# Performance work log

Measured on AMD Instinct MI355X. Metric: run time of the kernel, lower is better.

Reference implementation:

```python
import jax, jax.numpy as jnp
import numpy as np

B, N, F, D = 8, 2048, 128, 128


def setup_inputs() -> dict:
    key = jax.random.key(0)
    k1, k2, k3 = jax.random.split(key, 3)
    inputs = jax.random.normal(k1, (B, N, F), dtype=jnp.float32)
    adj = jax.random.uniform(k2, (B, N, N), dtype=jnp.float32)  # nonneg weights -> positive degrees
    W_kernel = jax.random.normal(k3, (F, D), dtype=jnp.float32) * (1.0 / np.sqrt(F))
    W_bias = jnp.zeros((D,), dtype=jnp.float32)
    return {"inputs": inputs, "adj": adj, "W_kernel": W_kernel, "W_bias": W_bias}


def _normalize_adjacency(adj):
    # D^{-1/2} A D^{-1/2}: same math as diag-matmul chain, via broadcast scaling
    d = jnp.sum(adj, axis=-1)                      # [B, N]
    d_sqrt_inv = jnp.power(d, -0.5)
    d_sqrt_inv = jnp.where(jnp.isinf(d_sqrt_inv), 0.0, d_sqrt_inv)
    return d_sqrt_inv[..., :, None] * adj * d_sqrt_inv[..., None, :]


def reference(inputs, adj, W_kernel, W_bias):
    adj_norm = _normalize_adjacency(adj)           # [B, N, N]
    feats = inputs @ W_kernel + W_bias             # [B, N, D]
    out = jnp.einsum('bnm,bmd->bnd', adj_norm, feats)
    return jax.nn.relu(out)
```

## Files before the change

### kernel.cpp

```cpp
#include <hip/hip_runtime.h>
#include <hip/hip_bf16.h>
#include <stdint.h>

#define B_ 8
#define N_ 2048
#define F_ 128
#define D_ 128

typedef short bf16x8 __attribute__((ext_vector_type(8)));
typedef float f32x4 __attribute__((ext_vector_type(4)));

__device__ __forceinline__ unsigned short f2bf(float f) {
    unsigned u = __float_as_uint(f);
    u += 0x7fffu + ((u >> 16) & 1u);
    return (unsigned short)(u >> 16);
}

__global__ __launch_bounds__(256) void k_degwt(const float* __restrict__ adj,
                                               const float* __restrict__ W,
                                               float* __restrict__ rs,
                                               unsigned short* __restrict__ Wt) {
    if (blockIdx.x < 4096) {
        const int wave = threadIdx.x >> 6, lane = threadIdx.x & 63;
        const int row = blockIdx.x * 4 + wave;
        const float4* p = (const float4*)(adj + (size_t)row * N_);
        float s = 0.f;
#pragma unroll
        for (int j = 0; j < 8; ++j) {
            float4 v = p[j * 64 + lane];
            s += (v.x + v.y) + (v.z + v.w);
        }
#pragma unroll
        for (int m = 1; m < 64; m <<= 1) s += __shfl_xor(s, m, 64);
        if (lane == 0) rs[row] = (s > 0.f) ? (1.0f / sqrtf(s)) : 0.f;
    } else {
        int c = (blockIdx.x - 4096) * 256 + threadIdx.x;
        int d = c >> 4, f0 = (c & 15) * 8;
        union { bf16x8 v; unsigned short u[8]; } pk;
#pragma unroll
        for (int e = 0; e < 8; ++e) pk.u[e] = f2bf(W[(size_t)(f0 + e) * D_ + d]);
        *(bf16x8*)(Wt + (size_t)d * F_ + f0) = pk.v;
    }
}

__global__ __launch_bounds__(256) void k_feat(const float* __restrict__ x,
                                              const unsigned short* __restrict__ Wt,
                                              const float* __restrict__ bias,
                                              unsigned short* __restrict__ gt) {
    __shared__ __align__(16) unsigned char sX[64 * 128 * 2];
    __shared__ __align__(16) unsigned char sW[128 * 128 * 2];
    const int t = threadIdx.x;
    const int R0 = blockIdx.x * 64;

#pragma unroll
    for (int j = 0; j < 8; ++j) {
        int c = j * 256 + t;
        unsigned L = (unsigned)c * 16u;
        unsigned lg = L ^ (((L >> 8) & 7u) << 4);
        const unsigned char* src = (const unsigned char*)Wt + lg;
        __builtin_amdgcn_global_load_lds(
            (const __attribute__((address_space(1))) void*)src,
            (__attribute__((address_space(3))) void*)(sW + L), 16, 0, 0);
    }
#pragma unroll
    for (int j = 0; j < 4; ++j) {
        int c = j * 256 + t;
        int row = c >> 4, sub = c & 15;
        const float4* src = (const float4*)(x + (size_t)(R0 + row) * F_ + sub * 8);
        float4 v0 = src[0], v1 = src[1];
        union { bf16x8 v; unsigned short u[8]; } pk;
        pk.u[0] = f2bf(v0.x); pk.u[1] = f2bf(v0.y); pk.u[2] = f2bf(v0.z); pk.u[3] = f2bf(v0.w);
        pk.u[4] = f2bf(v1.x); pk.u[5] = f2bf(v1.y); pk.u[6] = f2bf(v1.z); pk.u[7] = f2bf(v1.w);
        unsigned byte = (unsigned)(row * 256 + sub * 16);
        byte ^= ((byte >> 8) & 7u) << 4;
        *(bf16x8*)(sX + byte) = pk.v;
    }
    __syncthreads();

    const int w = t >> 6, l = t & 63, lr = l & 15, lh = l >> 4;
    f32x4 acc[8];
#pragma unroll
    for (int j = 0; j < 8; ++j) acc[j] = (f32x4){0.f, 0.f, 0.f, 0.f};

#pragma unroll
    for (int ks = 0; ks < 4; ++ks) {
        int f0 = lh * 8 + ks * 32;
        unsigned abyte = (unsigned)((w * 16 + lr) * 256 + f0 * 2);
        abyte ^= ((abyte >> 8) & 7u) << 4;
        bf16x8 a = *(const bf16x8*)(sX + abyte);
#pragma unroll
        for (int j = 0; j < 8; ++j) {
            unsigned bbyte = (unsigned)((j * 16 + lr) * 256 + f0 * 2);
            bbyte ^= ((bbyte >> 8) & 7u) << 4;
            bf16x8 bb = *(const bf16x8*)(sW + bbyte);
            acc[j] = __builtin_amdgcn_mfma_f32_16x16x32_bf16(a, bb, acc[j], 0, 0, 0);
        }
    }

#pragma unroll
    for (int j = 0; j < 8; ++j) {
        int d = j * 16 + lr;
        float bv = bias[d];
#pragma unroll
        for (int r = 0; r < 4; ++r) {
            int m = R0 + w * 16 + lh * 4 + r;
            float v = acc[j][r] + bv;
            int b = m >> 11, n = m & (N_ - 1);
            gt[((size_t)b * D_ + d) * N_ + n] = f2bf(v);
        }
    }
}

__global__ __launch_bounds__(512) void k_gcn(const float* __restrict__ adj,
                                             const unsigned short* __restrict__ gt,
                                             const float* __restrict__ rs,
                                             float* __restrict__ out) {
    __shared__ __align__(16) unsigned char sA[2][32 * 128 * 2];
    __shared__ __align__(16) unsigned char sB[2][128 * 128 * 2];

    unsigned bid = blockIdx.x;
    unsigned wg = (bid & 7u) * 64u + (bid >> 3);
    const int b = (int)(wg >> 6);
    const int nt = (int)(wg & 63u);
    const int R0 = nt * 32;

    const float* adjB = adj + (size_t)b * N_ * N_ + (size_t)R0 * N_;
    const unsigned short* gtB = gt + (size_t)b * D_ * N_;
    const float* rsB = rs + b * N_;

    const int t = threadIdx.x;
    const int w = t >> 6, l = t & 63, lr = l & 15, lh = l >> 4;
    const int wr = (w >> 2) * 16, wc = (w & 3) * 32;

    auto stage = [&](int bufidx, int k0) {
        unsigned char* sBb = sB[bufidx];
#pragma unroll
        for (int i = 0; i < 4; ++i) {
            int c = i * 512 + t;
            unsigned L = (unsigned)c * 16u;
            unsigned lg = L ^ (((L >> 8) & 7u) << 4);
            int d = (int)(lg >> 8);
            int mloc = (int)(lg & 255u) >> 1;
            const unsigned short* g = gtB + (size_t)d * N_ + k0 + mloc;
            __builtin_amdgcn_global_load_lds(
                (const __attribute__((address_space(1))) void*)g,
                (__attribute__((address_space(3))) void*)(sBb + L), 16, 0, 0);
        }
        {
            int row = t >> 4, sub = t & 15;
            const float4* src = (const float4*)(adjB + (size_t)row * N_ + k0 + sub * 8);
            const float4* rsm = (const float4*)(rsB + k0 + sub * 8);
            float4 v0 = src[0], v1 = src[1];
            float4 r0 = rsm[0], r1 = rsm[1];
            union { bf16x8 v; unsigned short u[8]; } pk;
            pk.u[0] = f2bf(v0.x * r0.x); pk.u[1] = f2bf(v0.y * r0.y);
            pk.u[2] = f2bf(v0.z * r0.z); pk.u[3] = f2bf(v0.w * r0.w);
            pk.u[4] = f2bf(v1.x * r1.x); pk.u[5] = f2bf(v1.y * r1.y);
            pk.u[6] = f2bf(v1.z * r1.z); pk.u[7] = f2bf(v1.w * r1.w);
            unsigned byte = (unsigned)(row * 256 + sub * 16);
            byte ^= ((byte >> 8) & 7u) << 4;
            *(bf16x8*)(sA[bufidx] + byte) = pk.v;
        }
    };

    f32x4 acc[2];
    acc[0] = (f32x4){0.f, 0.f, 0.f, 0.f};
    acc[1] = (f32x4){0.f, 0.f, 0.f, 0.f};

    stage(0, 0);
    __syncthreads();

    const int NITER = N_ / 128;
    for (int it = 0; it < NITER; ++it) {
        int cur = it & 1;
        if (it + 1 < NITER) stage(cur ^ 1, (it + 1) * 128);

        const unsigned char* pA = sA[cur];
        const unsigned char* pB = sB[cur];
#pragma unroll
        for (int kk = 0; kk < 4; ++kk) {
            unsigned abyte = (unsigned)((wr + lr) * 256 + lh * 16 + kk * 64);
            abyte ^= ((abyte >> 8) & 7u) << 4;
            bf16x8 a = *(const bf16x8*)(pA + abyte);
#pragma unroll
            for (int jn = 0; jn < 2; ++jn) {
                int d = wc + jn * 16 + lr;
                unsigned bbyte = (unsigned)(d * 256 + lh * 16 + kk * 64);
                bbyte ^= ((bbyte >> 8) & 7u) << 4;
                bf16x8 bb = *(const bf16x8*)(pB + bbyte);
                acc[jn] = __builtin_amdgcn_mfma_f32_16x16x32_bf16(a, bb, acc[jn], 0, 0, 0);
            }
        }
        __syncthreads();
    }

#pragma unroll
    for (int r = 0; r < 4; ++r) {
        int row = wr + lh * 4 + r;
        float rsn = rsB[R0 + row];
#pragma unroll
        for (int jn = 0; jn < 2; ++jn) {
            int d = wc + jn * 16 + lr;
            float v = acc[jn][r] * rsn;
            out[((size_t)(b * N_ + R0 + row)) * D_ + d] = fmaxf(v, 0.f);
        }
    }
}

extern "C" void kernel_launch(void* const* d_in, const int* in_sizes, int n_in,
                              void* d_out, int out_size, void* d_ws, size_t ws_size,
                              hipStream_t stream) {
    const float* inputs = (const float*)d_in[0];
    const float* adj    = (const float*)d_in[1];
    const float* Wk     = (const float*)d_in[2];
    const float* Wb     = (const float*)d_in[3];
    float* out = (float*)d_out;

    float* rs = (float*)d_ws;
    unsigned short* gt = (unsigned short*)((char*)d_ws + 65536);
    unsigned short* Wt = (unsigned short*)((char*)d_ws + 65536 + (size_t)B_ * D_ * N_ * 2);

    k_degwt<<<4096 + 8, 256, 0, stream>>>(adj, Wk, rs, Wt);
    k_feat <<<(B_ * N_) / 64, 256, 0, stream>>>(inputs, Wt, Wb, gt);
    k_gcn  <<<B_ * (N_ / 32), 512, 0, stream>>>(adj, gt, rs, out);
}
```

Measured before the change: 56.73 us.

## Fold column degree scaling into features and split K across waves in GCN matmul

The column-side D^{-1/2} scaling now happens once in the feature kernel, where it is applied to the projected features before they are stored as bf16. This removes the per-tile rs loads and multiplies from the adjacency staging path. The main kernel also changes its wave split: each wave now covers a 32x32 output tile over half of the K slice per iteration, loading two A and two B fragments for four MFMAs, which raises fragment reuse. The two K-halves are reduced through shared memory at the end, which adds an extra barrier and LDS traffic. Rounding to bf16 after scaling changes numerics slightly.

```diff
diff --git a/kernel.cpp b/kernel.cpp
--- a/kernel.cpp
+++ b/kernel.cpp
@@ -46,6 +46,7 @@
 __global__ __launch_bounds__(256) void k_feat(const float* __restrict__ x,
                                               const unsigned short* __restrict__ Wt,
                                               const float* __restrict__ bias,
+                                              const float* __restrict__ rs,
                                               unsigned short* __restrict__ gt) {
     __shared__ __align__(16) unsigned char sX[64 * 128 * 2];
     __shared__ __align__(16) unsigned char sW[128 * 128 * 2];
@@ -84,29 +85,30 @@
 
 #pragma unroll
     for (int ks = 0; ks < 4; ++ks) {
-        int f0 = lh * 8 + ks * 32;
-        unsigned abyte = (unsigned)((w * 16 + lr) * 256 + f0 * 2);
+        unsigned abyte = (unsigned)((w * 16 + lr) * 256 + lh * 16 + ks * 64);
         abyte ^= ((abyte >> 8) & 7u) << 4;
         bf16x8 a = *(const bf16x8*)(sX + abyte);
 #pragma unroll
         for (int j = 0; j < 8; ++j) {
-            unsigned bbyte = (unsigned)((j * 16 + lr) * 256 + f0 * 2);
+            unsigned bbyte = (unsigned)((j * 16 + lr) * 256 + lh * 16 + ks * 64);
             bbyte ^= ((bbyte >> 8) & 7u) << 4;
             bf16x8 bb = *(const bf16x8*)(sW + bbyte);
             acc[j] = __builtin_amdgcn_mfma_f32_16x16x32_bf16(a, bb, acc[j], 0, 0, 0);
         }
     }
 
+    const int m0 = R0 + w * 16 + lh * 4;
+    float4 r4 = *(const float4*)(rs + m0);
+    float rr[4] = {r4.x, r4.y, r4.z, r4.w};
 #pragma unroll
     for (int j = 0; j < 8; ++j) {
         int d = j * 16 + lr;
         float bv = bias[d];
 #pragma unroll
         for (int r = 0; r < 4; ++r) {
-            int m = R0 + w * 16 + lh * 4 + r;
-            float v = acc[j][r] + bv;
+            int m = m0 + r;
             int b = m >> 11, n = m & (N_ - 1);
-            gt[((size_t)b * D_ + d) * N_ + n] = f2bf(v);
+            gt[((size_t)b * D_ + d) * N_ + n] = f2bf((acc[j][r] + bv) * rr[r]);
         }
     }
 }
@@ -121,16 +123,15 @@
     unsigned bid = blockIdx.x;
     unsigned wg = (bid & 7u) * 64u + (bid >> 3);
     const int b = (int)(wg >> 6);
-    const int nt = (int)(wg & 63u);
-    const int R0 = nt * 32;
+    const int R0 = (int)(wg & 63u) * 32;
 
     const float* adjB = adj + (size_t)b * N_ * N_ + (size_t)R0 * N_;
     const unsigned short* gtB = gt + (size_t)b * D_ * N_;
-    const float* rsB = rs + b * N_;
+    const float* rsB = rs + (size_t)b * N_;
 
     const int t = threadIdx.x;
     const int w = t >> 6, l = t & 63, lr = l & 15, lh = l >> 4;
-    const int wr = (w >> 2) * 16, wc = (w & 3) * 32;
+    const int kg = w >> 2, cg = w & 3;
 
     auto stage = [&](int bufidx, int k0) {
         unsigned char* sBb = sB[bufidx];
@@ -149,23 +150,23 @@
         {
             int row = t >> 4, sub = t & 15;
             const float4* src = (const float4*)(adjB + (size_t)row * N_ + k0 + sub * 8);
-            const float4* rsm = (const float4*)(rsB + k0 + sub * 8);
             float4 v0 = src[0], v1 = src[1];
-            float4 r0 = rsm[0], r1 = rsm[1];
             union { bf16x8 v; unsigned short u[8]; } pk;
-            pk.u[0] = f2bf(v0.x * r0.x); pk.u[1] = f2bf(v0.y * r0.y);
-            pk.u[2] = f2bf(v0.z * r0.z); pk.u[3] = f2bf(v0.w * r0.w);
-            pk.u[4] = f2bf(v1.x * r1.x); pk.u[5] = f2bf(v1.y * r1.y);
-            pk.u[6] = f2bf(v1.z * r1.z); pk.u[7] = f2bf(v1.w * r1.w);
+            pk.u[0] = f2bf(v0.x); pk.u[1] = f2bf(v0.y);
+            pk.u[2] = f2bf(v0.z); pk.u[3] = f2bf(v0.w);
+            pk.u[4] = f2bf(v1.x); pk.u[5] = f2bf(v1.y);
+            pk.u[6] = f2bf(v1.z); pk.u[7] = f2bf(v1.w);
             unsigned byte = (unsigned)(row * 256 + sub * 16);
             byte ^= ((byte >> 8) & 7u) << 4;
             *(bf16x8*)(sA[bufidx] + byte) = pk.v;
         }
     };
 
-    f32x4 acc[2];
-    acc[0] = (f32x4){0.f, 0.f, 0.f, 0.f};
-    acc[1] = (f32x4){0.f, 0.f, 0.f, 0.f};
+    f32x4 acc[2][2];
+#pragma unroll
+    for (int i = 0; i < 2; ++i)
+#pragma unroll
+        for (int jn = 0; jn < 2; ++jn) acc[i][jn] = (f32x4){0.f, 0.f, 0.f, 0.f};
 
     stage(0, 0);
     __syncthreads();
@@ -178,31 +179,60 @@
         const unsigned char* pA = sA[cur];
         const unsigned char* pB = sB[cur];
 #pragma unroll
-        for (int kk = 0; kk < 4; ++kk) {
-            unsigned abyte = (unsigned)((wr + lr) * 256 + lh * 16 + kk * 64);
-            abyte ^= ((abyte >> 8) & 7u) << 4;
-            bf16x8 a = *(const bf16x8*)(pA + abyte);
+        for (int kk2 = 0; kk2 < 2; ++kk2) {
+            const int kk = kg * 2 + kk2;
+            bf16x8 a[2], bb[2];
+#pragma unroll
+            for (int i = 0; i < 2; ++i) {
+                unsigned byte = (unsigned)((i * 16 + lr) * 256 + lh * 16 + kk * 64);
+                byte ^= ((byte >> 8) & 7u) << 4;
+                a[i] = *(const bf16x8*)(pA + byte);
+            }
 #pragma unroll
             for (int jn = 0; jn < 2; ++jn) {
-                int d = wc + jn * 16 + lr;
-                unsigned bbyte = (unsigned)(d * 256 + lh * 16 + kk * 64);
-                bbyte ^= ((bbyte >> 8) & 7u) << 4;
-                bf16x8 bb = *(const bf16x8*)(pB + bbyte);
-                acc[jn] = __builtin_amdgcn_mfma_f32_16x16x32_bf16(a, bb, acc[jn], 0, 0, 0);
+                int d = cg * 32 + jn * 16 + lr;
+                unsigned byte = (unsigned)(d * 256 + lh * 16 + kk * 64);
+                byte ^= ((byte >> 8) & 7u) << 4;
+                bb[jn] = *(const bf16x8*)(pB + byte);
             }
+#pragma unroll
+            for (int i = 0; i < 2; ++i)
+#pragma unroll
+                for (int jn = 0; jn < 2; ++jn)
+                    acc[i][jn] = __builtin_amdgcn_mfma_f32_16x16x32_bf16(a[i], bb[jn], acc[i][jn], 0, 0, 0);
         }
         __syncthreads();
     }
 
-#pragma unroll
-    for (int r = 0; r < 4; ++r) {
-        int row = wr + lh * 4 + r;
-        float rsn = rsB[R0 + row];
-#pragma unroll
-        for (int jn = 0; jn < 2; ++jn) {
-            int d = wc + jn * 16 + lr;
-            float v = acc[jn][r] * rsn;
-            out[((size_t)(b * N_ + R0 + row)) * D_ + d] = fmaxf(v, 0.f);
+    float* sO = (float*)sA;
+    if (kg == 1) {
+#pragma unroll
+        for (int i = 0; i < 2; ++i)
+#pragma unroll
+            for (int jn = 0; jn < 2; ++jn)
+#pragma unroll
+                for (int r = 0; r < 4; ++r) {
+                    int rowl = i * 16 + lh * 4 + r;
+                    int d = cg * 32 + jn * 16 + lr;
+                    sO[rowl * 128 + d] = acc[i][jn][r];
+                }
+    }
+    __syncthreads();
+    if (kg == 0) {
+#pragma unroll
+        for (int i = 0; i < 2; ++i) {
+            float4 r4 = *(const float4*)(rsB + R0 + i * 16 + lh * 4);
+            float rr[4] = {r4.x, r4.y, r4.z, r4.w};
+#pragma unroll
+            for (int r = 0; r < 4; ++r) {
+                int rowl = i * 16 + lh * 4 + r;
+#pragma unroll
+                for (int jn = 0; jn < 2; ++jn) {
+                    int d = cg * 32 + jn * 16 + lr;
+                    float v = (acc[i][jn][r] + sO[rowl * 128 + d]) * rr[r];
+                    out[((size_t)(b * N_ + R0 + rowl)) * D_ + d] = fmaxf(v, 0.f);
+                }
+            }
         }
     }
 }
@@ -221,6 +251,6 @@
     unsigned short* Wt = (unsigned short*)((char*)d_ws + 65536 + (size_t)B_ * D_ * N_ * 2);
 
     k_degwt<<<4096 + 8, 256, 0, stream>>>(adj, Wk, rs, Wt);
-    k_feat <<<(B_ * N_) / 64, 256, 0, stream>>>(inputs, Wt, Wb, gt);
+    k_feat <<<(B_ * N_) / 64, 256, 0, stream>>>(inputs, Wt, Wb, rs, gt);
     k_gcn  <<<B_ * (N_ / 32), 512, 0, stream>>>(adj, gt, rs, out);
 }
```

New measurement: 55.64 us. No clear change (-1.9%).
